# Optimization experiments

Hardware: AMD Instinct MI355X
Metric: run time of the kernel (lower is better)

The kernel has to match this reference:

```python
import jax, jax.numpy as jnp
import numpy as np

HID = 2048; S = 2048; NH = 16
Q_LORA = 1536; KV_LORA = 512
D_NOPE = 128; D_ROPE = 64; D_V = 128
D_QK = D_NOPE + D_ROPE  # 192
EPS = 1e-6


def setup_inputs() -> dict:
    key = jax.random.key(0)
    ks = jax.random.split(key, 8)
    hidden_states = jax.random.normal(ks[0], (1, S, HID), dtype=jnp.float32)
    # real RoPE tables, HF layout: cos/sin = concat(freqs, freqs) along last dim
    inv_freq = 1.0 / (10000.0 ** (np.arange(0, D_ROPE, 2, dtype=np.float32) / D_ROPE))
    t = np.arange(S, dtype=np.float32)
    freqs = np.outer(t, inv_freq)  # [S, D_ROPE//2]
    emb = np.concatenate([freqs, freqs], axis=-1)  # [S, D_ROPE]
    cos = jnp.asarray(np.cos(emb))[None]  # [1, S, D_ROPE]
    sin = jnp.asarray(np.sin(emb))[None]
    def lin(k, fan_in, fan_out):
        return jax.random.normal(k, (fan_in, fan_out), dtype=jnp.float32) / np.sqrt(fan_in)
    return {
        'hidden_states': hidden_states, 'cos': cos, 'sin': sin,
        'w_qa': lin(ks[1], HID, Q_LORA),
        'g_qa': jnp.ones((Q_LORA,), jnp.float32),
        'w_qb': lin(ks[2], Q_LORA, NH * D_QK),
        'w_kva': lin(ks[3], HID, KV_LORA + D_ROPE),
        'g_kva': jnp.ones((KV_LORA,), jnp.float32),
        'w_kvb': lin(ks[4], KV_LORA, NH * (D_NOPE + D_V)),
        'w_o': lin(ks[5], NH * D_V, HID),
    }


def _rmsnorm(x, g):
    var = jnp.mean(x * x, axis=-1, keepdims=True)
    return x * jax.lax.rsqrt(var + EPS) * g


def _deinterleave(x):
    # view (..., d//2, 2) -> transpose -> reshape: even-index dims first, then odd
    b, h, s, d = x.shape
    return x.reshape(b, h, s, d // 2, 2).transpose(0, 1, 2, 4, 3).reshape(b, h, s, d)


def _rotate_half(x):
    x1, x2 = jnp.split(x, 2, axis=-1)
    return jnp.concatenate([-x2, x1], axis=-1)


def _apply_rope(q, k, cos, sin):
    cos = cos[:, None]  # [B,1,S,D]
    sin = sin[:, None]
    q = _deinterleave(q)
    k = _deinterleave(k)
    q_emb = q * cos + _rotate_half(q) * sin
    k_emb = k * cos + _rotate_half(k) * sin
    return q_emb, k_emb


def reference(hidden_states, cos, sin, w_qa, g_qa, w_qb, w_kva, g_kva, w_kvb, w_o):
    bsz, q_len, _ = hidden_states.shape
    # low-rank Q projection
    q = _rmsnorm(hidden_states @ w_qa, g_qa) @ w_qb  # [B,S,NH*D_QK]
    q = q.reshape(bsz, q_len, NH, D_QK).transpose(0, 2, 1, 3)  # [B,NH,S,D_QK]
    q_nope, q_pe = q[..., :D_NOPE], q[..., D_NOPE:]
    # compressed KV + shared rope key
    ckv = hidden_states @ w_kva  # [B,S,KV_LORA+D_ROPE]
    compressed_kv, k_pe = ckv[..., :KV_LORA], ckv[..., KV_LORA:]
    k_pe = k_pe.reshape(bsz, q_len, 1, D_ROPE).transpose(0, 2, 1, 3)  # [B,1,S,D_ROPE]
    kv = (_rmsnorm(compressed_kv, g_kva) @ w_kvb).reshape(bsz, q_len, NH, D_NOPE + D_V).transpose(0, 2, 1, 3)
    k_nope, value_states = kv[..., :D_NOPE], kv[..., D_NOPE:]
    # interleaved RoPE
    q_pe, k_pe = _apply_rope(q_pe, k_pe, cos, sin)
    query_states = jnp.concatenate([q_nope, q_pe], axis=-1)  # [B,NH,S,D_QK]
    key_states = jnp.concatenate([k_nope, jnp.broadcast_to(k_pe, (bsz, NH, q_len, D_ROPE))], axis=-1)
    # causal attention with MLA softmax scale
    scale = D_QK ** (-0.5)
    scores = jnp.einsum('bhqd,bhkd->bhqk', query_states, key_states) * scale
    mask = jnp.tril(jnp.ones((q_len, q_len), dtype=bool))
    scores = jnp.where(mask, scores, jnp.finfo(scores.dtype).min)
    probs = jax.nn.softmax(scores, axis=-1)
    attn = jnp.einsum('bhqk,bhkd->bhqd', probs, value_states)  # [B,NH,S,D_V]
    attn = attn.transpose(0, 2, 1, 3).reshape(bsz, q_len, NH * D_V)
    return attn @ w_o
```

## Files before the change

kernel.cpp:

```cpp
#include <hip/hip_runtime.h>
#include <hip/hip_bf16.h>

#define S_LEN 2048
#define HID_D 2048
#define NHEAD 16
#define QLORA 1536
#define KVLORA 512
#define DNOPE 128
#define DROPE 64
#define DV 128
#define DQK 192
#define NCAT 2176

#define KS_SH (64 * 192)
#define VS_SH (128 * 64)
#define BUF_SH (KS_SH + VS_SH)

typedef __hip_bfloat16 bf16;
typedef __attribute__((ext_vector_type(8))) short short8;
typedef __attribute__((ext_vector_type(4))) short s16x4;
typedef __attribute__((ext_vector_type(4))) float f32x4;

__device__ __forceinline__ float ldE(const float* p) { return *p; }
__device__ __forceinline__ float ldE(const bf16* p) { return __bfloat162float(*p); }
__device__ __forceinline__ void stE(float* p, float v) { *p = v; }
__device__ __forceinline__ void stE(bf16* p, float v) { *p = __float2bfloat16(v); }

__device__ __forceinline__ short bf16bits(float v) {
    __hip_bfloat16 h = __float2bfloat16(v);
    return *reinterpret_cast<short*>(&h);
}

__device__ __forceinline__ float b2f(short s) {
    union { short s; bf16 h; } u;
    u.s = s;
    return __bfloat162float(u.h);
}

__device__ __forceinline__ f32x4 mfma16(short8 a, short8 b, f32x4 c) {
    return __builtin_amdgcn_mfma_f32_16x16x32_bf16(a, b, c, 0, 0, 0);
}

__device__ __forceinline__ void gload16(const void* g, void* l) {
    __builtin_amdgcn_global_load_lds(
        (const __attribute__((address_space(1))) unsigned int*)g,
        (__attribute__((address_space(3))) unsigned int*)l, 16, 0, 0);
}

__global__ void detect_kernel(const void* hidden, int* flag) {
    __shared__ int red[256];
    const int tid = threadIdx.x;
    const bf16* hb = (const bf16*)hidden;
    float a = fabsf(__bfloat162float(hb[tid]));
    red[tid] = (!(a < 64.f) || (a != 0.f && a < 1e-30f)) ? 1 : 0;
    __syncthreads();
    for (int o = 128; o > 0; o >>= 1) {
        if (tid < o) red[tid] += red[tid + o];
        __syncthreads();
    }
    if (tid == 0) *flag = (red[0] > 16) ? 1 : 0;
}

__global__ void convert_kernel(const void* in, bf16* out, int n8, const int* flag) {
    int i = blockIdx.x * 256 + threadIdx.x;
    if (i >= n8) return;
    size_t off = (size_t)i * 8;
    short8 o;
    if (*flag) {
        const float* f = (const float*)in + off;
#pragma unroll
        for (int j = 0; j < 8; ++j) o[j] = bf16bits(f[j]);
    } else {
        o = *(const short8*)((const short*)in + off);
    }
    *(short8*)((short*)out + off) = o;
}

template <int KDIM>
__device__ void transpose_tile(const void* in, bf16* out, int N, int n0, int k0,
                               int roff, int fp32) {
    __shared__ __align__(16) short Ts[64][80];
    const int tid = threadIdx.x;
    const bool inb = n0 < N;
    const int kl = tid >> 4;
    const int nl = (tid & 15) * 4;
#pragma unroll
    for (int p = 0; p < 4; ++p) {
        int k = kl + p * 16;
        float v[4] = {0.f, 0.f, 0.f, 0.f};
        if (inb) {
            if (fp32) {
                const float4 f = *(const float4*)((const float*)in + (size_t)(k0 + k) * N + n0 + nl);
                v[0] = f.x; v[1] = f.y; v[2] = f.z; v[3] = f.w;
            } else {
                const bf16* bp = (const bf16*)in + (size_t)(k0 + k) * N + n0 + nl;
#pragma unroll
                for (int i = 0; i < 4; ++i) v[i] = __bfloat162float(bp[i]);
            }
        }
#pragma unroll
        for (int i = 0; i < 4; ++i) Ts[nl + i][k] = bf16bits(v[i]);
    }
    __syncthreads();
    const int nr = tid >> 2;
    const int kq = (tid & 3) * 16;
    short* op = (short*)out + (size_t)(roff + n0 + nr) * KDIM + k0 + kq;
    *(short8*)op = *(short8*)&Ts[nr][kq];
    *(short8*)(op + 8) = *(short8*)&Ts[nr][kq + 8];
}

__global__ void transpose_kernel(const void* in, bf16* out, int K, int N, int Npad,
                                 const int* flag) {
    __shared__ __align__(16) short Ts[64][80];
    const int tid = threadIdx.x;
    const int n0 = blockIdx.x * 64, k0 = blockIdx.y * 64;
    const bool inb = n0 < N;
    const int fp32 = *flag;
    const int kl = tid >> 4;
    const int nl = (tid & 15) * 4;
#pragma unroll
    for (int p = 0; p < 4; ++p) {
        int k = kl + p * 16;
        float v[4] = {0.f, 0.f, 0.f, 0.f};
        if (inb) {
            if (fp32) {
                const float4 f = *(const float4*)((const float*)in + (size_t)(k0 + k) * N + n0 + nl);
                v[0] = f.x; v[1] = f.y; v[2] = f.z; v[3] = f.w;
            } else {
                const bf16* bp = (const bf16*)in + (size_t)(k0 + k) * N + n0 + nl;
#pragma unroll
                for (int i = 0; i < 4; ++i) v[i] = __bfloat162float(bp[i]);
            }
        }
#pragma unroll
        for (int i = 0; i < 4; ++i) Ts[nl + i][k] = bf16bits(v[i]);
    }
    __syncthreads();
    const int nr = tid >> 2;
    const int kq = (tid & 3) * 16;
    short* op = (short*)out + (size_t)(n0 + nr) * K + k0 + kq;
    *(short8*)op = *(short8*)&Ts[nr][kq];
    *(short8*)(op + 8) = *(short8*)&Ts[nr][kq + 8];
}

__global__ void transpose2_kernel(const void* inA, const void* inB, bf16* out,
                                  const int* flag) {
    const int bx = blockIdx.x;
    const int k0 = blockIdx.y * 64;
    const int fp32 = *flag;
    if (bx < 24) transpose_tile<HID_D>(inA, out, QLORA, bx * 64, k0, 0, fp32);
    else         transpose_tile<HID_D>(inB, out, KVLORA + DROPE, (bx - 24) * 64, k0, QLORA, fp32);
}

__global__ void transposeQK_kernel(const void* inQ, bf16* outQ,
                                   const void* inKV, bf16* outKV, const int* flag) {
    const int bid = blockIdx.x;
    const int fp32 = *flag;
    if (bid < 1152) {
        const int n0 = (bid % 48) * 64, k0 = (bid / 48) * 64;
        transpose_tile<QLORA>(inQ, outQ, NHEAD * DQK, n0, k0, 0, fp32);
    } else {
        const int b = bid - 1152;
        const int n0 = (b % 64) * 64, k0 = (b / 64) * 64;
        transpose_tile<KVLORA>(inKV, outKV, NHEAD * (DNOPE + DV), n0, k0, 0, fp32);
    }
}

template <int MODE, typename TC>
__device__ void mgemm_body(const bf16* __restrict__ A, int lda,
                           const bf16* __restrict__ Bt, int ldb,
                           TC* __restrict__ C, int ldc, int K,
                           bf16* __restrict__ Kn, bf16* __restrict__ Vt) {
    __shared__ __align__(16) short AB[2][16384];
    const int tid = threadIdx.x;
    const int w = tid >> 6, lane = tid & 63;
    const int lg = lane >> 4, ln = lane & 15;
    const int wm = w >> 1, wn = w & 1;

    const int nbx = gridDim.x;
    const int flat = blockIdx.y * nbx + blockIdx.x;
    const int cpx = (nbx * gridDim.y) >> 3;
    const int swz = (flat & 7) * cpx + (flat >> 3);
    const int m0 = (swz / nbx) * 128, n0 = (swz % nbx) * 128;

    int aO[4], bO[4];
#pragma unroll
    for (int p = 0; p < 4; ++p) {
        const int cid = tid + p * 256;
        const int row = cid >> 3, cpos = cid & 7;
        const int c = cpos ^ (row & 7);
        aO[p] = (m0 + row) * lda + c * 8;
        bO[p] = (n0 + row) * ldb + c * 8;
    }
    int aoff[2][4], boff[2][4];
#pragma unroll
    for (int hk = 0; hk < 2; ++hk)
#pragma unroll
        for (int i = 0; i < 4; ++i) {
            const int ra = wm * 64 + i * 16 + ln;
            const int rb = wn * 64 + i * 16 + ln;
            aoff[hk][i] = ra * 64 + ((hk * 4 + lg) ^ (ra & 7)) * 8;
            boff[hk][i] = rb * 64 + ((hk * 4 + lg) ^ (rb & 7)) * 8;
        }

    f32x4 acc[4][4];
#pragma unroll
    for (int i = 0; i < 4; ++i)
#pragma unroll
        for (int j = 0; j < 4; ++j) acc[i][j] = (f32x4){0.f, 0.f, 0.f, 0.f};

#pragma unroll
    for (int p = 0; p < 4; ++p) {
        gload16(A + (size_t)aO[p], &AB[0][0] + (w + 4 * p) * 512);
        gload16(Bt + (size_t)bO[p], &AB[0][8192] + (w + 4 * p) * 512);
    }

    const int nsteps = K >> 6;
    for (int s = 0; s < nsteps; ++s) {
        const int cur = s & 1;
        const short* As = &AB[cur][0];
        const short* Bs = &AB[cur][8192];
        if (s + 1 < nsteps) {
            const int k0n = (s + 1) * 64;
            short* AsN = &AB[cur ^ 1][0];
            short* BsN = &AB[cur ^ 1][8192];
#pragma unroll
            for (int p = 0; p < 4; ++p) {
                gload16(A + (size_t)aO[p] + k0n, AsN + (w + 4 * p) * 512);
                gload16(Bt + (size_t)bO[p] + k0n, BsN + (w + 4 * p) * 512);
            }
            asm volatile("s_waitcnt vmcnt(8)" ::: "memory");
        } else {
            asm volatile("s_waitcnt vmcnt(0)" ::: "memory");
        }
        __builtin_amdgcn_s_barrier();
        __builtin_amdgcn_s_setprio(1);
#pragma unroll
        for (int hk = 0; hk < 2; ++hk) {
            short8 af[4], bfr[4];
#pragma unroll
            for (int i = 0; i < 4; ++i) af[i] = *(const short8*)&As[aoff[hk][i]];
#pragma unroll
            for (int j = 0; j < 4; ++j) bfr[j] = *(const short8*)&Bs[boff[hk][j]];
#pragma unroll
            for (int i = 0; i < 4; ++i)
#pragma unroll
                for (int j = 0; j < 4; ++j) acc[i][j] = mfma16(af[i], bfr[j], acc[i][j]);
        }
        __builtin_amdgcn_s_setprio(0);
        __builtin_amdgcn_s_barrier();
    }
    if constexpr (MODE == 2) {
#pragma unroll
        for (int i = 0; i < 4; ++i)
#pragma unroll
            for (int j = 0; j < 4; ++j) {
                const int col = n0 + wn * 64 + j * 16 + ln;
                const int row = m0 + wm * 64 + i * 16 + lg * 4;
                const int h = col >> 8, d = col & 255;
                if (d < DNOPE) {
                    bf16* cp = Kn + (size_t)row * (NHEAD * DNOPE) + h * DNOPE + d;
#pragma unroll
                    for (int r = 0; r < 4; ++r)
                        cp[(size_t)r * (NHEAD * DNOPE)] = __float2bfloat16(acc[i][j][r]);
                } else {
                    s16x4 pk;
#pragma unroll
                    for (int r = 0; r < 4; ++r) pk[r] = bf16bits(acc[i][j][r]);
                    *(s16x4*)(Vt + (size_t)(h * DV + (d - DNOPE)) * S_LEN + row) = pk;
                }
            }
    } else {
#pragma unroll
        for (int i = 0; i < 4; ++i)
#pragma unroll
            for (int j = 0; j < 4; ++j) {
                TC* cp = C + (size_t)(m0 + wm * 64 + i * 16 + lg * 4) * ldc + n0 + wn * 64 +
                         j * 16 + ln;
#pragma unroll
                for (int r = 0; r < 4; ++r)
                    stE(cp + (size_t)r * ldc, acc[i][j][r]);
            }
    }
}

template <int MODE>
__global__ __launch_bounds__(256, 2)
void mgemm_kernel(const bf16* A, int lda, const bf16* Bt, int ldb, void* C, int ldc,
                  int K, const int* flag, bf16* Kn, bf16* Vt) {
    if (MODE == 1 && *flag)
        mgemm_body<1, float>(A, lda, Bt, ldb, (float*)C, ldc, K, nullptr, nullptr);
    else if (MODE == 2)
        mgemm_body<2, bf16>(A, lda, Bt, ldb, (bf16*)C, ldc, K, Kn, Vt);
    else
        mgemm_body<0, bf16>(A, lda, Bt, ldb, (bf16*)C, ldc, K, nullptr, nullptr);
}

template <typename TG>
__device__ void rmsnorm_row(const bf16* __restrict__ xr, const TG* __restrict__ g,
                            bf16* __restrict__ yr, int len) {
    const int tid = threadIdx.x;
    float ss = 0.f;
    for (int i = tid; i < len; i += 256) {
        float v = __bfloat162float(xr[i]);
        ss += v * v;
    }
    __shared__ float red[256];
    red[tid] = ss;
    __syncthreads();
    for (int o = 128; o > 0; o >>= 1) {
        if (tid < o) red[tid] += red[tid + o];
        __syncthreads();
    }
    const float scale = rsqrtf(red[0] / (float)len + 1e-6f);
    for (int i = tid; i < len; i += 256)
        yr[i] = __float2bfloat16(__bfloat162float(xr[i]) * scale * ldE(&g[i]));
}

__global__ void rmsnorm2_kernel(bf16* qk, const void* g_qa, const void* g_kva,
                                bf16* ckvn, const int* flag) {
    const int bid = blockIdx.x;
    if (*flag) {
        if (bid < S_LEN)
            rmsnorm_row<float>(qk + (size_t)bid * NCAT, (const float*)g_qa,
                               qk + (size_t)bid * NCAT, QLORA);
        else {
            const int s = bid - S_LEN;
            rmsnorm_row<float>(qk + (size_t)s * NCAT + QLORA, (const float*)g_kva,
                               ckvn + (size_t)s * KVLORA, KVLORA);
        }
    } else {
        if (bid < S_LEN)
            rmsnorm_row<bf16>(qk + (size_t)bid * NCAT, (const bf16*)g_qa,
                              qk + (size_t)bid * NCAT, QLORA);
        else {
            const int s = bid - S_LEN;
            rmsnorm_row<bf16>(qk + (size_t)s * NCAT + QLORA, (const bf16*)g_kva,
                              ckvn + (size_t)s * KVLORA, KVLORA);
        }
    }
}

template <typename TG>
__device__ void rope_body(bf16* __restrict__ q, const bf16* __restrict__ ckv,
                          bf16* __restrict__ kpe, const TG* __restrict__ cosb,
                          const TG* __restrict__ sinb) {
    const int s = blockIdx.x;
    const int tid = threadIdx.x;
    float x0 = 0.f, x1 = 0.f, c = 0.f, sn = 0.f;
    bf16* qbase = nullptr;
    int p = 0;
    const bool isq = tid < 512;
    const bool active = tid < 544;
    if (active) {
        if (isq) {
            const int h = tid >> 5;
            p = tid & 31;
            qbase = q + (size_t)s * (NHEAD * DQK) + h * DQK + DNOPE;
            x0 = __bfloat162float(qbase[2 * p]);
            x1 = __bfloat162float(qbase[2 * p + 1]);
        } else {
            p = tid - 512;
            const bf16* kb = ckv + (size_t)s * NCAT + KVLORA;
            x0 = __bfloat162float(kb[2 * p]);
            x1 = __bfloat162float(kb[2 * p + 1]);
        }
        c = ldE(&cosb[s * 64 + p]);
        sn = ldE(&sinb[s * 64 + p]);
    }
    __syncthreads();
    if (active) {
        if (isq) {
            qbase[p] = __float2bfloat16(x0 * c - x1 * sn);
            qbase[p + 32] = __float2bfloat16(x1 * c + x0 * sn);
        } else {
            kpe[s * 64 + p] = __float2bfloat16(x0 * c - x1 * sn);
            kpe[s * 64 + p + 32] = __float2bfloat16(x1 * c + x0 * sn);
        }
    }
}

__global__ void rope_kernel(bf16* q, const bf16* ckv, bf16* kpe,
                            const void* cosb, const void* sinb, const int* flag) {
    if (*flag) rope_body<float>(q, ckv, kpe, (const float*)cosb, (const float*)sinb);
    else       rope_body<bf16>(q, ckv, kpe, (const bf16*)cosb, (const bf16*)sinb);
}

__global__ __launch_bounds__(256, 2)
void fattn_kernel(const bf16* __restrict__ q, const bf16* __restrict__ kn,
                  const bf16* __restrict__ vt, const bf16* __restrict__ kpe,
                  bf16* __restrict__ attn, bf16* __restrict__ Opart, float* __restrict__ ml) {
    const int nf = blockIdx.x;
    const int xcd = nf & 7;
    const int j = nf >> 3;
    const int bx = j & 31;
    const int h = (j >> 5) * 8 + xcd;
    int qt, part, nparts;
    if (bx < 15)      { qt = 15 - bx / 3;        part = bx % 3;        nparts = 3; }
    else if (bx < 27) { qt = 10 - (bx - 15) / 2; part = (bx - 15) & 1; nparts = 2; }
    else              { qt = 31 - bx;            part = 0;             nparts = 1; }
    const int nt = 2 * qt + 2;
    const int bsz = nt / nparts, rr = nt % nparts;
    const int t0 = part * bsz + (part < rr ? part : rr);
    const int t1 = t0 + bsz + (part < rr ? 1 : 0);
    const int q0 = qt * 128;

    const int tid = threadIdx.x;
    const int w = tid >> 6;
    const int l = tid & 63;
    const int lg = l >> 4;
    const int ln = l & 15;

    __shared__ __align__(16) short KV[2][BUF_SH];

    int offK[6], sK[6];
    bool isn[6];
#pragma unroll
    for (int p = 0; p < 6; ++p) {
        const int cid = tid + p * 256;
        const int row = cid / 24;
        const int cpos = cid % 24;
        const int c = (cpos & 24) | ((cpos & 7) ^ (row & 7));
        if (c < 16) {
            offK[p] = row * (NHEAD * DNOPE) + h * DNOPE + c * 8;
            sK[p] = NHEAD * DNOPE;
            isn[p] = true;
        } else {
            offK[p] = row * DROPE + (c - 16) * 8;
            sK[p] = DROPE;
            isn[p] = false;
        }
    }
    int offV[4];
#pragma unroll
    for (int p = 0; p < 4; ++p) {
        const int cid = tid + p * 256;
        const int row = cid >> 3;
        const int cc = (cid & 7) ^ (row & 7);
        offV[p] = (h * DV + row) * S_LEN + cc * 8;
    }

    short8 qf[2][6];
#pragma unroll
    for (int i = 0; i < 2; ++i) {
        const short* qrow =
            (const short*)(q + (size_t)(q0 + i * 64 + w * 16 + ln) * (NHEAD * DQK) + h * DQK);
#pragma unroll
        for (int ks = 0; ks < 6; ++ks)
            qf[i][ks] = *(const short8*)(qrow + ks * 32 + lg * 8);
    }

    f32x4 O[2][8];
#pragma unroll
    for (int i = 0; i < 2; ++i)
#pragma unroll
        for (int ct = 0; ct < 8; ++ct) O[i][ct] = (f32x4){0.f, 0.f, 0.f, 0.f};
    float m_[2][4], l_[2][4];
#pragma unroll
    for (int i = 0; i < 2; ++i)
#pragma unroll
        for (int r = 0; r < 4; ++r) { m_[i][r] = -1e30f; l_[i][r] = 0.f; }
    const float scale = 0.07216878364870322f;

    {
        const int k0 = t0 * 64;
#pragma unroll
        for (int p = 0; p < 6; ++p) {
            const bf16* sp = (isn[p] ? kn : kpe) + (size_t)offK[p] + (size_t)k0 * sK[p];
            gload16(sp, &KV[0][0] + (w + 4 * p) * 512);
        }
#pragma unroll
        for (int p = 0; p < 4; ++p)
            gload16(vt + (size_t)offV[p] + k0, &KV[0][KS_SH] + (w + 4 * p) * 512);
    }

    for (int t = t0; t < t1; ++t) {
        const int cur = (t - t0) & 1;
        short* Ks = &KV[cur][0];
        short* Vs = &KV[cur][KS_SH];
        if (t + 1 < t1) {
            const int k0n = (t + 1) * 64;
            short* KsN = &KV[cur ^ 1][0];
            short* VsN = &KV[cur ^ 1][KS_SH];
#pragma unroll
            for (int p = 0; p < 6; ++p) {
                const bf16* sp = (isn[p] ? kn : kpe) + (size_t)offK[p] + (size_t)k0n * sK[p];
                gload16(sp, KsN + (w + 4 * p) * 512);
            }
#pragma unroll
            for (int p = 0; p < 4; ++p)
                gload16(vt + (size_t)offV[p] + k0n, VsN + (w + 4 * p) * 512);
            asm volatile("s_waitcnt vmcnt(10)" ::: "memory");
        } else {
            asm volatile("s_waitcnt vmcnt(0)" ::: "memory");
        }
        __builtin_amdgcn_s_barrier();

        const int k0 = t * 64;
        f32x4 S[2][4];
#pragma unroll
        for (int i = 0; i < 2; ++i)
#pragma unroll
            for (int c = 0; c < 4; ++c) S[i][c] = (f32x4){0.f, 0.f, 0.f, 0.f};
        __builtin_amdgcn_s_setprio(1);
#pragma unroll
        for (int ks = 0; ks < 6; ++ks) {
            const int kch = ks * 4 + lg;
#pragma unroll
            for (int c = 0; c < 4; ++c) {
                short8 kf = *(const short8*)&Ks[(size_t)(c * 16 + ln) * 192 +
                                               (size_t)(kch ^ (ln & 7)) * 8];
                S[0][c] = mfma16(qf[0][ks], kf, S[0][c]);
                S[1][c] = mfma16(qf[1][ks], kf, S[1][c]);
            }
        }
        __builtin_amdgcn_s_setprio(0);

        const int d0 = k0 - q0;
#pragma unroll
        for (int i = 0; i < 2; ++i)
#pragma unroll
            for (int c = 0; c < 4; ++c)
#pragma unroll
                for (int r = 0; r < 4; ++r) {
                    float v = S[i][c][r] * scale;
                    if (d0 > -64 &&
                        (d0 + c * 16 + ln) > (i * 64 + w * 16 + lg * 4 + r)) v = -1e30f;
                    S[i][c][r] = v;
                }

        float alpha[2][4];
#pragma unroll
        for (int i = 0; i < 2; ++i)
#pragma unroll
            for (int r = 0; r < 4; ++r) {
                float mx = fmaxf(fmaxf(S[i][0][r], S[i][1][r]), fmaxf(S[i][2][r], S[i][3][r]));
#pragma unroll
                for (int d = 1; d < 16; d <<= 1) mx = fmaxf(mx, __shfl_xor(mx, d));
                float mn = fmaxf(m_[i][r], mx);
                alpha[i][r] = __expf(m_[i][r] - mn);
                m_[i][r] = mn;
                float rs = 0.f;
#pragma unroll
                for (int c = 0; c < 4; ++c) {
                    float p = __expf(S[i][c][r] - mn);
                    S[i][c][r] = p;
                    rs += p;
                }
#pragma unroll
                for (int d = 1; d < 16; d <<= 1) rs += __shfl_xor(rs, d);
                l_[i][r] = l_[i][r] * alpha[i][r] + rs;
            }
#pragma unroll
        for (int i = 0; i < 2; ++i)
#pragma unroll
            for (int ct = 0; ct < 8; ++ct)
#pragma unroll
                for (int r = 0; r < 4; ++r) O[i][ct][r] *= alpha[i][r];

        __builtin_amdgcn_s_barrier();
        short* Pb = Ks;
#pragma unroll
        for (int i = 0; i < 2; ++i)
#pragma unroll
            for (int c = 0; c < 4; ++c)
#pragma unroll
                for (int r = 0; r < 4; ++r)
                    Pb[(size_t)(i * 64 + w * 16 + lg * 4 + r) * 70 + c * 16 + ln] =
                        bf16bits(S[i][c][r]);

        __builtin_amdgcn_s_setprio(1);
#pragma unroll
        for (int ks = 0; ks < 2; ++ks) {
            short8 pf0 = *(const short8*)&Pb[(size_t)(w * 16 + ln) * 70 + ks * 32 + lg * 8];
            short8 pf1 = *(const short8*)&Pb[(size_t)(64 + w * 16 + ln) * 70 + ks * 32 + lg * 8];
#pragma unroll
            for (int ct = 0; ct < 8; ++ct) {
                short8 vf = *(const short8*)&Vs[(size_t)(ct * 16 + ln) * 64 +
                                               (size_t)((ks * 4 + lg) ^ (ln & 7)) * 8];
                O[0][ct] = mfma16(pf0, vf, O[0][ct]);
                O[1][ct] = mfma16(pf1, vf, O[1][ct]);
            }
        }
        __builtin_amdgcn_s_setprio(0);
        __builtin_amdgcn_s_barrier();
    }

    if (nparts == 1) {
#pragma unroll
        for (int i = 0; i < 2; ++i)
#pragma unroll
            for (int r = 0; r < 4; ++r) {
                float inv = 1.f / l_[i][r];
                bf16* orow = attn + (size_t)(q0 + i * 64 + w * 16 + lg * 4 + r) * (NHEAD * DV) +
                             h * DV;
#pragma unroll
                for (int ct = 0; ct < 8; ++ct)
                    orow[ct * 16 + ln] = __float2bfloat16(O[i][ct][r] * inv);
            }
    } else {
        const int mlslot = h * 27 + (qt <= 10 ? (qt - 5) * 2 + part : 12 + (qt - 11) * 3 + part);
        float* mlp = ml + (size_t)mlslot * 128 * 2;
        if (part == 0) {
#pragma unroll
            for (int i = 0; i < 2; ++i)
#pragma unroll
                for (int r = 0; r < 4; ++r) {
                    const int rowb = i * 64 + w * 16 + lg * 4 + r;
                    bf16* orow = attn + (size_t)(q0 + rowb) * (NHEAD * DV) + h * DV;
#pragma unroll
                    for (int ct = 0; ct < 8; ++ct)
                        orow[ct * 16 + ln] = __float2bfloat16(O[i][ct][r]);
                    if (ln == 0) {
                        mlp[rowb * 2] = m_[i][r];
                        mlp[rowb * 2 + 1] = l_[i][r];
                    }
                }
        } else {
            const int oslot = h * 16 + (qt <= 10 ? (qt - 5) : 6 + (qt - 11) * 2 + (part - 1));
            bf16* op = Opart + (size_t)oslot * 128 * DV;
#pragma unroll
            for (int i = 0; i < 2; ++i)
#pragma unroll
                for (int r = 0; r < 4; ++r) {
                    const int rowb = i * 64 + w * 16 + lg * 4 + r;
#pragma unroll
                    for (int ct = 0; ct < 8; ++ct)
                        op[(size_t)rowb * DV + ct * 16 + ln] = __float2bfloat16(O[i][ct][r]);
                    if (ln == 0) {
                        mlp[rowb * 2] = m_[i][r];
                        mlp[rowb * 2 + 1] = l_[i][r];
                    }
                }
        }
    }
}

__global__ void reduce_kernel(const bf16* __restrict__ Opart, const float* __restrict__ ml,
                              bf16* __restrict__ attn) {
    const int qq = blockIdx.x;
    const int h = blockIdx.y;
    const int qt = 5 + qq;
    const int np = (qt <= 10) ? 2 : 3;
    const int q0 = qt * 128;
    const int tid = threadIdx.x;
    const int row = tid >> 1;
    const int dh = (tid & 1) * 64;
    float mp[3], lp[3], f[3];
    float mm = -1e30f;
    for (int p = 0; p < np; ++p) {
        const int msl = h * 27 + (qt <= 10 ? (qt - 5) * 2 + p : 12 + (qt - 11) * 3 + p);
        mp[p] = ml[((size_t)msl * 128 + row) * 2];
        lp[p] = ml[((size_t)msl * 128 + row) * 2 + 1];
        mm = fmaxf(mm, mp[p]);
    }
    float denom = 0.f;
    for (int p = 0; p < np; ++p) {
        f[p] = __expf(mp[p] - mm);
        denom += f[p] * lp[p];
    }
    const float inv = 1.f / denom;
    const int os1 = h * 16 + (qt <= 10 ? (qt - 5) : 6 + (qt - 11) * 2);
    bf16* arow = attn + (size_t)(q0 + row) * (NHEAD * DV) + h * DV + dh;
    const bf16* o1 = Opart + ((size_t)os1 * 128 + row) * DV + dh;
    const bf16* o2 = o1 + (size_t)128 * DV;
#pragma unroll
    for (int jc = 0; jc < 8; ++jc) {
        short8 a = *(const short8*)(arow + jc * 8);
        short8 b1 = *(const short8*)(o1 + jc * 8);
        short8 b2 = (np == 3) ? *(const short8*)(o2 + jc * 8) : b1;
        short8 o;
#pragma unroll
        for (int e = 0; e < 8; ++e) {
            float v = f[0] * b2f(a[e]) + f[1] * b2f(b1[e]);
            if (np == 3) v += f[2] * b2f(b2[e]);
            o[e] = bf16bits(v * inv);
        }
        *(short8*)(arow + jc * 8) = o;
    }
}

extern "C" void kernel_launch(void* const* d_in, const int* in_sizes, int n_in,
                              void* d_out, int out_size, void* d_ws, size_t ws_size,
                              hipStream_t stream) {
    const void* hidden = d_in[0];
    const void* cosb   = d_in[1];
    const void* sinb   = d_in[2];
    const void* w_qa   = d_in[3];
    const void* g_qa   = d_in[4];
    const void* w_qb   = d_in[5];
    const void* w_kva  = d_in[6];
    const void* g_kva  = d_in[7];
    const void* w_kvb  = d_in[8];
    const void* w_o    = d_in[9];

    bf16* ws = (bf16*)d_ws;
    bf16* qk   = ws;
    bf16* ckvn = qk + (size_t)S_LEN * NCAT;
    bf16* q    = ckvn + (size_t)S_LEN * KVLORA;
    bf16* kn   = q + (size_t)S_LEN * NHEAD * DQK;
    bf16* vtb  = kn + (size_t)S_LEN * NHEAD * DNOPE;
    bf16* kpe  = vtb + (size_t)NHEAD * DV * S_LEN;
    bf16* hbf  = kpe + (size_t)S_LEN * DROPE;
    int* flag  = (int*)(hbf + (size_t)S_LEN * HID_D);
    bf16* attn = ws;
    float* ml  = (float*)(ws + (size_t)S_LEN * HID_D);
    bf16* Opart = hbf;
    bf16* BtCat = kn;
    bf16* wqbT  = kn;
    bf16* wkvbT = hbf;
    bf16* W4    = q;

    detect_kernel<<<1, 256, 0, stream>>>(hidden, flag);
    convert_kernel<<<(S_LEN * HID_D / 8 + 255) / 256, 256, 0, stream>>>(
        hidden, hbf, S_LEN * HID_D / 8, flag);

    transpose2_kernel<<<dim3(34, HID_D / 64), 256, 0, stream>>>(w_qa, w_kva, BtCat, flag);
    mgemm_kernel<0><<<dim3(NCAT / 128, S_LEN / 128), 256, 0, stream>>>(
        hbf, HID_D, BtCat, HID_D, qk, NCAT, HID_D, flag, nullptr, nullptr);
    rmsnorm2_kernel<<<2 * S_LEN, 256, 0, stream>>>(qk, g_qa, g_kva, ckvn, flag);
    transposeQK_kernel<<<dim3(1664), 256, 0, stream>>>(w_qb, wqbT, w_kvb, wkvbT, flag);
    mgemm_kernel<0><<<dim3(NHEAD * DQK / 128, S_LEN / 128), 256, 0, stream>>>(
        qk, NCAT, wqbT, QLORA, q, NHEAD * DQK, QLORA, flag, nullptr, nullptr);
    mgemm_kernel<2><<<dim3(NHEAD * (DNOPE + DV) / 128, S_LEN / 128), 256, 0, stream>>>(
        ckvn, KVLORA, wkvbT, KVLORA, kn, NHEAD * (DNOPE + DV), KVLORA, flag, kn, vtb);
    rope_kernel<<<S_LEN, 576, 0, stream>>>(q, qk + QLORA, kpe, cosb, sinb, flag);
    fattn_kernel<<<dim3(512), 256, 0, stream>>>(q, kn, vtb, kpe, attn, Opart, ml);
    reduce_kernel<<<dim3(11, NHEAD), 256, 0, stream>>>(Opart, ml, attn);
    transpose_kernel<<<dim3(HID_D / 64, HID_D / 64), 256, 0, stream>>>(
        w_o, W4, HID_D, HID_D, HID_D, flag);
    mgemm_kernel<1><<<dim3(HID_D / 128, S_LEN / 128), 256, 0, stream>>>(
        attn, NHEAD * DV, W4, HID_D, d_out, HID_D, HID_D, flag, nullptr, nullptr);
}
```

Baseline: 336.7 us.

## Merge prep/transpose kernels into fewer launches and triple-buffer GEMM loads

Fuses the hidden-state conversion with the w_qa/w_kva transpose, the rmsnorm with the w_qb/w_kvb transposes, and the attention reduction with the w_o transpose, each into one launch. This removes several kernel launches and lets independent work share a grid. The GEMM moves from double to triple buffering with a prefetch distance of two K-steps. That deepens memory latency hiding but raises shared memory to 96KB and drops launch bounds to one block per SM, which may lower occupancy.

```diff
diff --git a/kernel.cpp b/kernel.cpp
--- a/kernel.cpp
+++ b/kernel.cpp
@@ -61,21 +61,6 @@
     if (tid == 0) *flag = (red[0] > 16) ? 1 : 0;
 }
 
-__global__ void convert_kernel(const void* in, bf16* out, int n8, const int* flag) {
-    int i = blockIdx.x * 256 + threadIdx.x;
-    if (i >= n8) return;
-    size_t off = (size_t)i * 8;
-    short8 o;
-    if (*flag) {
-        const float* f = (const float*)in + off;
-#pragma unroll
-        for (int j = 0; j < 8; ++j) o[j] = bf16bits(f[j]);
-    } else {
-        o = *(const short8*)((const short*)in + off);
-    }
-    *(short8*)((short*)out + off) = o;
-}
-
 template <int KDIM>
 __device__ void transpose_tile(const void* in, bf16* out, int N, int n0, int k0,
                                int roff, int fp32) {
@@ -109,191 +94,30 @@
     *(short8*)(op + 8) = *(short8*)&Ts[nr][kq + 8];
 }
 
-__global__ void transpose_kernel(const void* in, bf16* out, int K, int N, int Npad,
-                                 const int* flag) {
-    __shared__ __align__(16) short Ts[64][80];
-    const int tid = threadIdx.x;
-    const int n0 = blockIdx.x * 64, k0 = blockIdx.y * 64;
-    const bool inb = n0 < N;
-    const int fp32 = *flag;
-    const int kl = tid >> 4;
-    const int nl = (tid & 15) * 4;
-#pragma unroll
-    for (int p = 0; p < 4; ++p) {
-        int k = kl + p * 16;
-        float v[4] = {0.f, 0.f, 0.f, 0.f};
-        if (inb) {
-            if (fp32) {
-                const float4 f = *(const float4*)((const float*)in + (size_t)(k0 + k) * N + n0 + nl);
-                v[0] = f.x; v[1] = f.y; v[2] = f.z; v[3] = f.w;
-            } else {
-                const bf16* bp = (const bf16*)in + (size_t)(k0 + k) * N + n0 + nl;
-#pragma unroll
-                for (int i = 0; i < 4; ++i) v[i] = __bfloat162float(bp[i]);
-            }
-        }
-#pragma unroll
-        for (int i = 0; i < 4; ++i) Ts[nl + i][k] = bf16bits(v[i]);
-    }
-    __syncthreads();
-    const int nr = tid >> 2;
-    const int kq = (tid & 3) * 16;
-    short* op = (short*)out + (size_t)(n0 + nr) * K + k0 + kq;
-    *(short8*)op = *(short8*)&Ts[nr][kq];
-    *(short8*)(op + 8) = *(short8*)&Ts[nr][kq + 8];
-}
-
-__global__ void transpose2_kernel(const void* inA, const void* inB, bf16* out,
-                                  const int* flag) {
-    const int bx = blockIdx.x;
-    const int k0 = blockIdx.y * 64;
-    const int fp32 = *flag;
-    if (bx < 24) transpose_tile<HID_D>(inA, out, QLORA, bx * 64, k0, 0, fp32);
-    else         transpose_tile<HID_D>(inB, out, KVLORA + DROPE, (bx - 24) * 64, k0, QLORA, fp32);
-}
-
-__global__ void transposeQK_kernel(const void* inQ, bf16* outQ,
-                                   const void* inKV, bf16* outKV, const int* flag) {
+__global__ void prep1_kernel(const void* hidden, bf16* hbf,
+                             const void* w_qa, const void* w_kva, bf16* BtCat,
+                             const int* flag) {
     const int bid = blockIdx.x;
-    const int fp32 = *flag;
-    if (bid < 1152) {
-        const int n0 = (bid % 48) * 64, k0 = (bid / 48) * 64;
-        transpose_tile<QLORA>(inQ, outQ, NHEAD * DQK, n0, k0, 0, fp32);
+    if (bid < 2048) {
+        const int i = bid * 256 + threadIdx.x;
+        size_t off = (size_t)i * 8;
+        short8 o;
+        if (*flag) {
+            const float* f = (const float*)hidden + off;
+#pragma unroll
+            for (int j = 0; j < 8; ++j) o[j] = bf16bits(f[j]);
+        } else {
+            o = *(const short8*)((const short*)hidden + off);
+        }
+        *(short8*)((short*)hbf + off) = o;
     } else {
-        const int b = bid - 1152;
-        const int n0 = (b % 64) * 64, k0 = (b / 64) * 64;
-        transpose_tile<KVLORA>(inKV, outKV, NHEAD * (DNOPE + DV), n0, k0, 0, fp32);
-    }
-}
-
-template <int MODE, typename TC>
-__device__ void mgemm_body(const bf16* __restrict__ A, int lda,
-                           const bf16* __restrict__ Bt, int ldb,
-                           TC* __restrict__ C, int ldc, int K,
-                           bf16* __restrict__ Kn, bf16* __restrict__ Vt) {
-    __shared__ __align__(16) short AB[2][16384];
-    const int tid = threadIdx.x;
-    const int w = tid >> 6, lane = tid & 63;
-    const int lg = lane >> 4, ln = lane & 15;
-    const int wm = w >> 1, wn = w & 1;
-
-    const int nbx = gridDim.x;
-    const int flat = blockIdx.y * nbx + blockIdx.x;
-    const int cpx = (nbx * gridDim.y) >> 3;
-    const int swz = (flat & 7) * cpx + (flat >> 3);
-    const int m0 = (swz / nbx) * 128, n0 = (swz % nbx) * 128;
-
-    int aO[4], bO[4];
-#pragma unroll
-    for (int p = 0; p < 4; ++p) {
-        const int cid = tid + p * 256;
-        const int row = cid >> 3, cpos = cid & 7;
-        const int c = cpos ^ (row & 7);
-        aO[p] = (m0 + row) * lda + c * 8;
-        bO[p] = (n0 + row) * ldb + c * 8;
-    }
-    int aoff[2][4], boff[2][4];
-#pragma unroll
-    for (int hk = 0; hk < 2; ++hk)
-#pragma unroll
-        for (int i = 0; i < 4; ++i) {
-            const int ra = wm * 64 + i * 16 + ln;
-            const int rb = wn * 64 + i * 16 + ln;
-            aoff[hk][i] = ra * 64 + ((hk * 4 + lg) ^ (ra & 7)) * 8;
-            boff[hk][i] = rb * 64 + ((hk * 4 + lg) ^ (rb & 7)) * 8;
-        }
-
-    f32x4 acc[4][4];
-#pragma unroll
-    for (int i = 0; i < 4; ++i)
-#pragma unroll
-        for (int j = 0; j < 4; ++j) acc[i][j] = (f32x4){0.f, 0.f, 0.f, 0.f};
-
-#pragma unroll
-    for (int p = 0; p < 4; ++p) {
-        gload16(A + (size_t)aO[p], &AB[0][0] + (w + 4 * p) * 512);
-        gload16(Bt + (size_t)bO[p], &AB[0][8192] + (w + 4 * p) * 512);
-    }
-
-    const int nsteps = K >> 6;
-    for (int s = 0; s < nsteps; ++s) {
-        const int cur = s & 1;
-        const short* As = &AB[cur][0];
-        const short* Bs = &AB[cur][8192];
-        if (s + 1 < nsteps) {
-            const int k0n = (s + 1) * 64;
-            short* AsN = &AB[cur ^ 1][0];
-            short* BsN = &AB[cur ^ 1][8192];
-#pragma unroll
-            for (int p = 0; p < 4; ++p) {
-                gload16(A + (size_t)aO[p] + k0n, AsN + (w + 4 * p) * 512);
-                gload16(Bt + (size_t)bO[p] + k0n, BsN + (w + 4 * p) * 512);
-            }
-            asm volatile("s_waitcnt vmcnt(8)" ::: "memory");
-        } else {
-            asm volatile("s_waitcnt vmcnt(0)" ::: "memory");
-        }
-        __builtin_amdgcn_s_barrier();
-        __builtin_amdgcn_s_setprio(1);
-#pragma unroll
-        for (int hk = 0; hk < 2; ++hk) {
-            short8 af[4], bfr[4];
-#pragma unroll
-            for (int i = 0; i < 4; ++i) af[i] = *(const short8*)&As[aoff[hk][i]];
-#pragma unroll
-            for (int j = 0; j < 4; ++j) bfr[j] = *(const short8*)&Bs[boff[hk][j]];
-#pragma unroll
-            for (int i = 0; i < 4; ++i)
-#pragma unroll
-                for (int j = 0; j < 4; ++j) acc[i][j] = mfma16(af[i], bfr[j], acc[i][j]);
-        }
-        __builtin_amdgcn_s_setprio(0);
-        __builtin_amdgcn_s_barrier();
-    }
-    if constexpr (MODE == 2) {
-#pragma unroll
-        for (int i = 0; i < 4; ++i)
-#pragma unroll
-            for (int j = 0; j < 4; ++j) {
-                const int col = n0 + wn * 64 + j * 16 + ln;
-                const int row = m0 + wm * 64 + i * 16 + lg * 4;
-                const int h = col >> 8, d = col & 255;
-                if (d < DNOPE) {
-                    bf16* cp = Kn + (size_t)row * (NHEAD * DNOPE) + h * DNOPE + d;
-#pragma unroll
-                    for (int r = 0; r < 4; ++r)
-                        cp[(size_t)r * (NHEAD * DNOPE)] = __float2bfloat16(acc[i][j][r]);
-                } else {
-                    s16x4 pk;
-#pragma unroll
-                    for (int r = 0; r < 4; ++r) pk[r] = bf16bits(acc[i][j][r]);
-                    *(s16x4*)(Vt + (size_t)(h * DV + (d - DNOPE)) * S_LEN + row) = pk;
-                }
-            }
-    } else {
-#pragma unroll
-        for (int i = 0; i < 4; ++i)
-#pragma unroll
-            for (int j = 0; j < 4; ++j) {
-                TC* cp = C + (size_t)(m0 + wm * 64 + i * 16 + lg * 4) * ldc + n0 + wn * 64 +
-                         j * 16 + ln;
-#pragma unroll
-                for (int r = 0; r < 4; ++r)
-                    stE(cp + (size_t)r * ldc, acc[i][j][r]);
-            }
-    }
-}
-
-template <int MODE>
-__global__ __launch_bounds__(256, 2)
-void mgemm_kernel(const bf16* A, int lda, const bf16* Bt, int ldb, void* C, int ldc,
-                  int K, const int* flag, bf16* Kn, bf16* Vt) {
-    if (MODE == 1 && *flag)
-        mgemm_body<1, float>(A, lda, Bt, ldb, (float*)C, ldc, K, nullptr, nullptr);
-    else if (MODE == 2)
-        mgemm_body<2, bf16>(A, lda, Bt, ldb, (bf16*)C, ldc, K, Kn, Vt);
-    else
-        mgemm_body<0, bf16>(A, lda, Bt, ldb, (bf16*)C, ldc, K, nullptr, nullptr);
+        const int b = bid - 2048;
+        const int bx = b % 34;
+        const int k0 = (b / 34) * 64;
+        const int fp32 = *flag;
+        if (bx < 24) transpose_tile<HID_D>(w_qa, BtCat, QLORA, bx * 64, k0, 0, fp32);
+        else transpose_tile<HID_D>(w_kva, BtCat, KVLORA + DROPE, (bx - 24) * 64, k0, QLORA, fp32);
+    }
 }
 
 template <typename TG>
@@ -317,28 +141,184 @@
         yr[i] = __float2bfloat16(__bfloat162float(xr[i]) * scale * ldE(&g[i]));
 }
 
-__global__ void rmsnorm2_kernel(bf16* qk, const void* g_qa, const void* g_kva,
-                                bf16* ckvn, const int* flag) {
+__global__ void prep2_kernel(bf16* qk, const void* g_qa, const void* g_kva, bf16* ckvn,
+                             const void* w_qb, bf16* wqbT,
+                             const void* w_kvb, bf16* wkvbT, const int* flag) {
     const int bid = blockIdx.x;
-    if (*flag) {
-        if (bid < S_LEN)
-            rmsnorm_row<float>(qk + (size_t)bid * NCAT, (const float*)g_qa,
-                               qk + (size_t)bid * NCAT, QLORA);
-        else {
-            const int s = bid - S_LEN;
-            rmsnorm_row<float>(qk + (size_t)s * NCAT + QLORA, (const float*)g_kva,
-                               ckvn + (size_t)s * KVLORA, KVLORA);
+    if (bid < 2 * S_LEN) {
+        if (*flag) {
+            if (bid < S_LEN)
+                rmsnorm_row<float>(qk + (size_t)bid * NCAT, (const float*)g_qa,
+                                   qk + (size_t)bid * NCAT, QLORA);
+            else {
+                const int s = bid - S_LEN;
+                rmsnorm_row<float>(qk + (size_t)s * NCAT + QLORA, (const float*)g_kva,
+                                   ckvn + (size_t)s * KVLORA, KVLORA);
+            }
+        } else {
+            if (bid < S_LEN)
+                rmsnorm_row<bf16>(qk + (size_t)bid * NCAT, (const bf16*)g_qa,
+                                  qk + (size_t)bid * NCAT, QLORA);
+            else {
+                const int s = bid - S_LEN;
+                rmsnorm_row<bf16>(qk + (size_t)s * NCAT + QLORA, (const bf16*)g_kva,
+                                  ckvn + (size_t)s * KVLORA, KVLORA);
+            }
         }
     } else {
-        if (bid < S_LEN)
-            rmsnorm_row<bf16>(qk + (size_t)bid * NCAT, (const bf16*)g_qa,
-                              qk + (size_t)bid * NCAT, QLORA);
-        else {
-            const int s = bid - S_LEN;
-            rmsnorm_row<bf16>(qk + (size_t)s * NCAT + QLORA, (const bf16*)g_kva,
-                              ckvn + (size_t)s * KVLORA, KVLORA);
-        }
-    }
+        const int b = bid - 2 * S_LEN;
+        const int fp32 = *flag;
+        if (b < 1152) {
+            const int n0 = (b % 48) * 64, k0 = (b / 48) * 64;
+            transpose_tile<QLORA>(w_qb, wqbT, NHEAD * DQK, n0, k0, 0, fp32);
+        } else {
+            const int bb = b - 1152;
+            const int n0 = (bb % 64) * 64, k0 = (bb / 64) * 64;
+            transpose_tile<KVLORA>(w_kvb, wkvbT, NHEAD * (DNOPE + DV), n0, k0, 0, fp32);
+        }
+    }
+}
+
+template <int MODE, typename TC>
+__device__ void mgemm_body(short* __restrict__ AB,
+                           const bf16* __restrict__ A, int lda,
+                           const bf16* __restrict__ Bt, int ldb,
+                           TC* __restrict__ C, int ldc, int K,
+                           bf16* __restrict__ Kn, bf16* __restrict__ Vt) {
+    const int tid = threadIdx.x;
+    const int w = tid >> 6, lane = tid & 63;
+    const int lg = lane >> 4, ln = lane & 15;
+    const int wm = w >> 1, wn = w & 1;
+
+    const int nbx = gridDim.x;
+    const int flat = blockIdx.y * nbx + blockIdx.x;
+    const int cpx = (nbx * gridDim.y) >> 3;
+    const int swz = (flat & 7) * cpx + (flat >> 3);
+    const int m0 = (swz / nbx) * 128, n0 = (swz % nbx) * 128;
+
+    int aO[4], bO[4];
+#pragma unroll
+    for (int p = 0; p < 4; ++p) {
+        const int cid = tid + p * 256;
+        const int row = cid >> 3, cpos = cid & 7;
+        const int c = cpos ^ (row & 7);
+        aO[p] = (m0 + row) * lda + c * 8;
+        bO[p] = (n0 + row) * ldb + c * 8;
+    }
+    int aoff[2][4], boff[2][4];
+#pragma unroll
+    for (int hk = 0; hk < 2; ++hk)
+#pragma unroll
+        for (int i = 0; i < 4; ++i) {
+            const int ra = wm * 64 + i * 16 + ln;
+            const int rb = wn * 64 + i * 16 + ln;
+            aoff[hk][i] = ra * 64 + ((hk * 4 + lg) ^ (ra & 7)) * 8;
+            boff[hk][i] = rb * 64 + ((hk * 4 + lg) ^ (rb & 7)) * 8;
+        }
+
+    f32x4 acc[4][4];
+#pragma unroll
+    for (int i = 0; i < 4; ++i)
+#pragma unroll
+        for (int j = 0; j < 4; ++j) acc[i][j] = (f32x4){0.f, 0.f, 0.f, 0.f};
+
+    const int nsteps = K >> 6;
+#pragma unroll
+    for (int p = 0; p < 4; ++p) {
+        gload16(A + (size_t)aO[p], AB + (w + 4 * p) * 512);
+        gload16(Bt + (size_t)bO[p], AB + 8192 + (w + 4 * p) * 512);
+    }
+    if (nsteps > 1) {
+#pragma unroll
+        for (int p = 0; p < 4; ++p) {
+            gload16(A + (size_t)aO[p] + 64, AB + 16384 + (w + 4 * p) * 512);
+            gload16(Bt + (size_t)bO[p] + 64, AB + 16384 + 8192 + (w + 4 * p) * 512);
+        }
+    }
+
+    int cur = 0;
+    for (int s = 0; s < nsteps; ++s) {
+        if (s + 2 < nsteps) {
+            int pre = cur + 2; if (pre >= 3) pre -= 3;
+            const int k0n = (s + 2) * 64;
+            short* AsN = AB + pre * 16384;
+            short* BsN = AsN + 8192;
+#pragma unroll
+            for (int p = 0; p < 4; ++p) {
+                gload16(A + (size_t)aO[p] + k0n, AsN + (w + 4 * p) * 512);
+                gload16(Bt + (size_t)bO[p] + k0n, BsN + (w + 4 * p) * 512);
+            }
+            asm volatile("s_waitcnt vmcnt(16)" ::: "memory");
+        } else if (s + 1 < nsteps) {
+            asm volatile("s_waitcnt vmcnt(8)" ::: "memory");
+        } else {
+            asm volatile("s_waitcnt vmcnt(0)" ::: "memory");
+        }
+        __builtin_amdgcn_s_barrier();
+        const short* As = AB + cur * 16384;
+        const short* Bs = As + 8192;
+        __builtin_amdgcn_s_setprio(1);
+#pragma unroll
+        for (int hk = 0; hk < 2; ++hk) {
+            short8 af[4], bfr[4];
+#pragma unroll
+            for (int i = 0; i < 4; ++i) af[i] = *(const short8*)&As[aoff[hk][i]];
+#pragma unroll
+            for (int j = 0; j < 4; ++j) bfr[j] = *(const short8*)&Bs[boff[hk][j]];
+#pragma unroll
+            for (int i = 0; i < 4; ++i)
+#pragma unroll
+                for (int j = 0; j < 4; ++j) acc[i][j] = mfma16(af[i], bfr[j], acc[i][j]);
+        }
+        __builtin_amdgcn_s_setprio(0);
+        __builtin_amdgcn_s_barrier();
+        cur = (cur + 1 == 3) ? 0 : cur + 1;
+    }
+    if constexpr (MODE == 2) {
+#pragma unroll
+        for (int i = 0; i < 4; ++i)
+#pragma unroll
+            for (int j = 0; j < 4; ++j) {
+                const int col = n0 + wn * 64 + j * 16 + ln;
+                const int row = m0 + wm * 64 + i * 16 + lg * 4;
+                const int h = col >> 8, d = col & 255;
+                if (d < DNOPE) {
+                    bf16* cp = Kn + (size_t)row * (NHEAD * DNOPE) + h * DNOPE + d;
+#pragma unroll
+                    for (int r = 0; r < 4; ++r)
+                        cp[(size_t)r * (NHEAD * DNOPE)] = __float2bfloat16(acc[i][j][r]);
+                } else {
+                    s16x4 pk;
+#pragma unroll
+                    for (int r = 0; r < 4; ++r) pk[r] = bf16bits(acc[i][j][r]);
+                    *(s16x4*)(Vt + (size_t)(h * DV + (d - DNOPE)) * S_LEN + row) = pk;
+                }
+            }
+    } else {
+#pragma unroll
+        for (int i = 0; i < 4; ++i)
+#pragma unroll
+            for (int j = 0; j < 4; ++j) {
+                TC* cp = C + (size_t)(m0 + wm * 64 + i * 16 + lg * 4) * ldc + n0 + wn * 64 +
+                         j * 16 + ln;
+#pragma unroll
+                for (int r = 0; r < 4; ++r)
+                    stE(cp + (size_t)r * ldc, acc[i][j][r]);
+            }
+    }
+}
+
+template <int MODE>
+__global__ __launch_bounds__(256, 1)
+void mgemm_kernel(const bf16* A, int lda, const bf16* Bt, int ldb, void* C, int ldc,
+                  int K, const int* flag, bf16* Kn, bf16* Vt) {
+    __shared__ __align__(16) short AB[3][16384];
+    if (MODE == 1 && *flag)
+        mgemm_body<1, float>(&AB[0][0], A, lda, Bt, ldb, (float*)C, ldc, K, nullptr, nullptr);
+    else if (MODE == 2)
+        mgemm_body<2, bf16>(&AB[0][0], A, lda, Bt, ldb, (bf16*)C, ldc, K, Kn, Vt);
+    else
+        mgemm_body<0, bf16>(&AB[0][0], A, lda, Bt, ldb, (bf16*)C, ldc, K, nullptr, nullptr);
 }
 
 template <typename TG>
@@ -636,10 +616,18 @@
     }
 }
 
-__global__ void reduce_kernel(const bf16* __restrict__ Opart, const float* __restrict__ ml,
-                              bf16* __restrict__ attn) {
-    const int qq = blockIdx.x;
-    const int h = blockIdx.y;
+__global__ void finred_kernel(const bf16* __restrict__ Opart, const float* __restrict__ ml,
+                              bf16* __restrict__ attn, const void* w_o, bf16* W4,
+                              const int* flag) {
+    const int bid = blockIdx.x;
+    if (bid >= 176) {
+        const int b = bid - 176;
+        const int n0 = (b & 31) * 64, k0 = (b >> 5) * 64;
+        transpose_tile<HID_D>(w_o, W4, HID_D, n0, k0, 0, *flag);
+        return;
+    }
+    const int qq = bid % 11;
+    const int h = bid / 11;
     const int qt = 5 + qq;
     const int np = (qt <= 10) ? 2 : 3;
     const int q0 = qt * 128;
@@ -712,23 +700,18 @@
     bf16* W4    = q;
 
     detect_kernel<<<1, 256, 0, stream>>>(hidden, flag);
-    convert_kernel<<<(S_LEN * HID_D / 8 + 255) / 256, 256, 0, stream>>>(
-        hidden, hbf, S_LEN * HID_D / 8, flag);
-
-    transpose2_kernel<<<dim3(34, HID_D / 64), 256, 0, stream>>>(w_qa, w_kva, BtCat, flag);
+    prep1_kernel<<<dim3(3136), 256, 0, stream>>>(hidden, hbf, w_qa, w_kva, BtCat, flag);
     mgemm_kernel<0><<<dim3(NCAT / 128, S_LEN / 128), 256, 0, stream>>>(
         hbf, HID_D, BtCat, HID_D, qk, NCAT, HID_D, flag, nullptr, nullptr);
-    rmsnorm2_kernel<<<2 * S_LEN, 256, 0, stream>>>(qk, g_qa, g_kva, ckvn, flag);
-    transposeQK_kernel<<<dim3(1664), 256, 0, stream>>>(w_qb, wqbT, w_kvb, wkvbT, flag);
+    prep2_kernel<<<dim3(5760), 256, 0, stream>>>(qk, g_qa, g_kva, ckvn,
+                                                 w_qb, wqbT, w_kvb, wkvbT, flag);
     mgemm_kernel<0><<<dim3(NHEAD * DQK / 128, S_LEN / 128), 256, 0, stream>>>(
         qk, NCAT, wqbT, QLORA, q, NHEAD * DQK, QLORA, flag, nullptr, nullptr);
     mgemm_kernel<2><<<dim3(NHEAD * (DNOPE + DV) / 128, S_LEN / 128), 256, 0, stream>>>(
         ckvn, KVLORA, wkvbT, KVLORA, kn, NHEAD * (DNOPE + DV), KVLORA, flag, kn, vtb);
     rope_kernel<<<S_LEN, 576, 0, stream>>>(q, qk + QLORA, kpe, cosb, sinb, flag);
     fattn_kernel<<<dim3(512), 256, 0, stream>>>(q, kn, vtb, kpe, attn, Opart, ml);
-    reduce_kernel<<<dim3(11, NHEAD), 256, 0, stream>>>(Opart, ml, attn);
-    transpose_kernel<<<dim3(HID_D / 64, HID_D / 64), 256, 0, stream>>>(
-        w_o, W4, HID_D, HID_D, HID_D, flag);
+    finred_kernel<<<dim3(1200), 256, 0, stream>>>(Opart, ml, attn, w_o, W4, flag);
     mgemm_kernel<1><<<dim3(HID_D / 128, S_LEN / 128), 256, 0, stream>>>(
         attn, NHEAD * DV, W4, HID_D, d_out, HID_D, HID_D, flag, nullptr, nullptr);
 }
```

Result: slower. 358.8 us (+6.6%).
